# Optimization experiments

Hardware: AMD Instinct MI355X
Metric: run time of the kernel (lower is better)

## Reference

```python
import jax, jax.numpy as jnp
import numpy as np

B, T, S, H = 8, 256, 256, 512


def setup_inputs() -> dict:
    key = jax.random.key(0)
    k1, k2, k3, k4, k5, k6, k7 = jax.random.split(key, 7)
    query = jax.random.normal(k1, (B, T, H), dtype=jnp.float32)
    encoder_outputs = jax.random.normal(k2, (B, S, H), dtype=jnp.float32)
    src_lengths = jax.random.randint(k3, (B,), 1, S + 1)
    src_lengths = src_lengths.at[0].set(S)  # ensure max(lengths) == S (torch code masks to lengths.max())
    scale = 1.0 / np.sqrt(H)
    W_s = jax.random.normal(k4, (H, H), dtype=jnp.float32) * scale      # nn.Linear(H,H) weight
    W_h = jax.random.normal(k5, (H, H), dtype=jnp.float32) * scale
    v = jax.random.normal(k6, (H,), dtype=jnp.float32) * scale          # nn.Linear(H,1) weight
    W_out = jax.random.normal(k7, (H, 2 * H), dtype=jnp.float32) * scale  # nn.Linear(2H,H) weight
    return {"query": query, "encoder_outputs": encoder_outputs, "src_lengths": src_lengths,
            "W_s": W_s, "W_h": W_h, "v": v, "W_out": W_out}


def reference(query, encoder_outputs, src_lengths, W_s, W_h, v, W_out):
    # torch Linear: y = x @ W.T
    Ws_q = jnp.einsum('bth,oh->bto', query, W_s)            # (B,T,H)
    Wh_e = jnp.einsum('bsh,oh->bso', encoder_outputs, W_h)  # (B,S,H)
    # score(i,j) = v^T tanh(Ws_q_j + Wh_e_i), broadcast over (B,T,S,H)
    energies = jnp.einsum('btsh,h->bts',
                          jnp.tanh(Ws_q[:, :, None, :] + Wh_e[:, None, :, :]), v)
    mask = jnp.arange(encoder_outputs.shape[1]) < src_lengths[:, None]  # (B,S)
    energies = jnp.where(mask[:, None, :], energies, -jnp.inf)
    attn_weights = jax.nn.softmax(energies, axis=-1)        # (B,T,S)
    context = jnp.einsum('bts,bsh->bth', attn_weights, encoder_outputs)
    combined = jnp.concatenate([context, query], axis=-1)   # (B,T,2H)
    attn_out = jnp.tanh(jnp.einsum('btk,ok->bto', combined, W_out))
    return attn_out
```

## Files before the change

### kernel.cpp

```cpp
#include <hip/hip_runtime.h>
#include <hip/hip_bf16.h>


typedef __attribute__((ext_vector_type(8))) short bf16x8;
typedef __attribute__((ext_vector_type(4))) float floatx4;

#define C2LOG2E 2.8853900817779268f
#define LOG2E   1.4426950408889634f
#define NEGBIG  -1e30f

__device__ __forceinline__ float fexp2(float x) { return __builtin_amdgcn_exp2f(x); }
__device__ __forceinline__ float frcp(float x)  { return __builtin_amdgcn_rcpf(x); }
__device__ __forceinline__ float ftanh(float x) {
    return 1.0f - 2.0f * frcp(1.0f + fexp2(C2LOG2E * x));
}

__device__ __forceinline__ unsigned int f2bf_bits(float f) {
    unsigned int u = __float_as_uint(f);
    return (u + 0x7fffu + ((u >> 16) & 1u)) >> 16;
}

__global__ __launch_bounds__(256) void cast_all_bf16(
    const float* __restrict__ q,  const float* __restrict__ e,
    const float* __restrict__ Ws, const float* __restrict__ Wh,
    const float* __restrict__ Wo,
    unsigned short* __restrict__ qb,  unsigned short* __restrict__ eb,
    unsigned short* __restrict__ Wsb, unsigned short* __restrict__ Whb,
    unsigned short* __restrict__ Wob)
{
    int blk = blockIdx.x;
    const float* src; unsigned short* dst; int base;
    if      (blk < 1024) { src = q;  dst = qb;  base = blk; }
    else if (blk < 2048) { src = e;  dst = eb;  base = blk - 1024; }
    else if (blk < 2304) { src = Ws; dst = Wsb; base = blk - 2048; }
    else if (blk < 2560) { src = Wh; dst = Whb; base = blk - 2304; }
    else                 { src = Wo; dst = Wob; base = blk - 2560; }
    size_t i = (size_t)base * 1024 + threadIdx.x * 4;
    float4 f = *(const float4*)(src + i);
    ushort4 o;
    o.x = (unsigned short)f2bf_bits(f.x);
    o.y = (unsigned short)f2bf_bits(f.y);
    o.z = (unsigned short)f2bf_bits(f.z);
    o.w = (unsigned short)f2bf_bits(f.w);
    *(ushort4*)(dst + i) = o;
}

__global__ __launch_bounds__(256) void gemm32x64_tanh_dual(
    const unsigned short* __restrict__ Xa, const unsigned short* __restrict__ Wa,
    float* __restrict__ Ca,
    const unsigned short* __restrict__ Xb, const unsigned short* __restrict__ Wb_,
    float* __restrict__ Cb)
{
    __shared__ unsigned short sA[32 * 72];
    __shared__ unsigned short sB[64 * 72];
    const int K = 512;
    int blk = blockIdx.x;
    const unsigned short* X; const unsigned short* W; float* C;
    int mt, nt, N;
    if (blk < 512) { X = Xa; W = Wa; C = Ca; N = 512;  mt = blk >> 3; nt = blk & 7; }
    else { blk -= 512; X = Xb; W = Wb_; C = Cb; N = 2048; mt = blk >> 5; nt = blk & 31; }
    int row0 = mt * 32, col0 = nt * 64;
    int tid = threadIdx.x, lane = tid & 63, w = tid >> 6;
    int srA = tid >> 3, scA = (tid & 7) * 8;
    int srB = tid >> 2, scB = (tid & 3) * 16;
    int mw = (w & 1) * 16, nw = (w >> 1) * 32;
    int r = lane & 15, kq = (lane >> 4) * 8;

    floatx4 acc0 = {0,0,0,0}, acc1 = {0,0,0,0};
    const unsigned short* ga = X + (size_t)(row0 + srA) * K + scA;
    const unsigned short* gb = W + (size_t)(col0 + srB) * K + scB;

    for (int kb = 0; kb < 8; ++kb) {
        uint4 a0 = *(const uint4*)(ga);
        uint4 b0 = *(const uint4*)(gb);
        uint4 b1 = *(const uint4*)(gb + 8);
        ga += 64; gb += 64;
        __syncthreads();
        *(uint4*)&sA[srA * 72 + scA]     = a0;
        *(uint4*)&sB[srB * 72 + scB]     = b0;
        *(uint4*)&sB[srB * 72 + scB + 8] = b1;
        __syncthreads();
#pragma unroll
        for (int ks = 0; ks < 64; ks += 32) {
            bf16x8 af  = *(const bf16x8*)&sA[(mw + r) * 72 + ks + kq];
            bf16x8 bf0 = *(const bf16x8*)&sB[(nw + r) * 72 + ks + kq];
            bf16x8 bf1 = *(const bf16x8*)&sB[(nw + 16 + r) * 72 + ks + kq];
            acc0 = __builtin_amdgcn_mfma_f32_16x16x32_bf16(af, bf0, acc0, 0, 0, 0);
            acc1 = __builtin_amdgcn_mfma_f32_16x16x32_bf16(af, bf1, acc1, 0, 0, 0);
        }
    }
    int rq = (lane >> 4) * 4;
    float* cp = C + (size_t)(row0 + mw + rq) * N + col0 + nw + r;
#pragma unroll
    for (int i = 0; i < 4; ++i) {
        cp[(size_t)i * N]      = ftanh(acc0[i]);
        cp[(size_t)i * N + 16] = ftanh(acc1[i]);
    }
}

#define TQ 4
__global__ __launch_bounds__(512) void energies_softmax(
    const float* __restrict__ Aq,
    const float* __restrict__ BhT,
    const float* __restrict__ Vv,
    const int* __restrict__ Len,
    unsigned short* __restrict__ Wb)
{
    __shared__ float sA[TQ][512];
    __shared__ float sV[512];
    __shared__ float sRed[8][TQ][257];
    __shared__ float sE[TQ][256];

    int tid  = threadIdx.x;
    int lane = tid & 63;
    int w    = tid >> 6;
    int blk  = blockIdx.x;
    int b    = blk >> 6;
    int tq   = blk & 63;
    int row0g = b * 256 + tq * TQ;
    int len  = Len[b];
    int jmax = (len + 63) >> 6;

    {
        int idx = tid * 4, t = idx >> 9, c = idx & 511;
        *(float4*)&sA[t][c] = *(const float4*)(Aq + (size_t)(row0g + t) * 512 + c);
    }
    sV[tid] = Vv[tid];
    __syncthreads();

    int h0 = w * 64;
    float acc[TQ][4] = {{0.f}};
    const float* bt = BhT + (size_t)h0 * 2048 + b * 256 + lane;

#pragma unroll 2
    for (int hh = 0; hh < 64; hh += 4) {
        float Bv[4][4];
#pragma unroll
        for (int i = 0; i < 4; ++i)
#pragma unroll
            for (int j = 0; j < 4; ++j)
                if (j < jmax) Bv[i][j] = bt[(size_t)(hh + i) * 2048 + 64 * j];
        float4 v4 = *(const float4*)&sV[h0 + hh];
#pragma unroll
        for (int t = 0; t < TQ; ++t) {
            float4 a4 = *(const float4*)&sA[t][h0 + hh];
#pragma unroll
            for (int j = 0; j < 4; ++j) {
                if (j < jmax) {
                    float n0 = a4.x + Bv[0][j], n1 = a4.y + Bv[1][j];
                    float n2 = a4.z + Bv[2][j], n3 = a4.w + Bv[3][j];
                    float d0 = fmaf(a4.x, Bv[0][j], 1.0f), d1 = fmaf(a4.y, Bv[1][j], 1.0f);
                    float d2 = fmaf(a4.z, Bv[2][j], 1.0f), d3 = fmaf(a4.w, Bv[3][j], 1.0f);
                    float x0 = v4.x * n0, x1 = v4.y * n1;
                    float x2 = v4.z * n2, x3 = v4.w * n3;
                    float num01 = fmaf(x1, d0, x0 * d1);
                    float num23 = fmaf(x3, d2, x2 * d3);
                    acc[t][j] = fmaf(num01, frcp(d0 * d1), acc[t][j]);
                    acc[t][j] = fmaf(num23, frcp(d2 * d3), acc[t][j]);
                }
            }
        }
    }

#pragma unroll
    for (int t = 0; t < TQ; ++t)
#pragma unroll
        for (int j = 0; j < 4; ++j)
            sRed[w][t][lane + 64 * j] = acc[t][j];
    __syncthreads();
#pragma unroll
    for (int rep = 0; rep < 2; ++rep) {
        int p = tid + rep * 512;
        int t = p >> 8, s = p & 255;
        float sum = 0.f;
#pragma unroll
        for (int ww = 0; ww < 8; ++ww) sum += sRed[ww][t][s];
        sE[t][s] = sum;
    }
    __syncthreads();

    if (w < TQ) {
        float ev[4];
#pragma unroll
        for (int j = 0; j < 4; ++j) {
            int s = lane + 64 * j;
            ev[j] = (s < len) ? sE[w][s] : NEGBIG;
        }
        float m = fmaxf(fmaxf(ev[0], ev[1]), fmaxf(ev[2], ev[3]));
#pragma unroll
        for (int o = 1; o < 64; o <<= 1) m = fmaxf(m, __shfl_xor(m, o, 64));
        float wv[4], wsum = 0.f;
#pragma unroll
        for (int j = 0; j < 4; ++j) { wv[j] = fexp2((ev[j] - m) * LOG2E); wsum += wv[j]; }
#pragma unroll
        for (int o = 1; o < 64; o <<= 1) wsum += __shfl_xor(wsum, o, 64);
        float inv = frcp(wsum);
        unsigned short* wrow = Wb + (size_t)(row0g + w) * 256;
#pragma unroll
        for (int j = 0; j < 4; ++j)
            wrow[lane + 64 * j] = (unsigned short)f2bf_bits(wv[j] * inv);
    }
}

__global__ __launch_bounds__(512) void ctx_gemm(
    const unsigned short* __restrict__ Wbw,
    const unsigned short* __restrict__ Eb,
    unsigned short* __restrict__ Ctx)
{
    __shared__ unsigned short EncT[64][264];
    __shared__ unsigned short sWb[64][264];
    int tid = threadIdx.x, lane = tid & 63, w = tid >> 6;
    int blk = blockIdx.x;
    int b = blk & 7, hq = (blk >> 3) & 7, tg = blk >> 6;

    {
        int s = tid >> 1, hg = (tid & 1) * 32;
        const ushort4* src = (const ushort4*)(Eb + (size_t)(b * 256 + s) * 512 + hq * 64 + hg);
#pragma unroll
        for (int k = 0; k < 8; ++k) {
            ushort4 u = src[k];
            EncT[hg + k * 4 + 0][s] = u.x;
            EncT[hg + k * 4 + 1][s] = u.y;
            EncT[hg + k * 4 + 2][s] = u.z;
            EncT[hg + k * 4 + 3][s] = u.w;
        }
    }
    {
        int row = tid >> 3, seg = (tid & 7) * 32;
        const ushort4* src = (const ushort4*)(Wbw + (size_t)(b * 256 + tg * 64 + row) * 256 + seg);
        ushort4* dst = (ushort4*)&sWb[row][seg];
#pragma unroll
        for (int k = 0; k < 8; ++k) dst[k] = src[k];
    }
    __syncthreads();

    int mt = w & 3, npair = w >> 2;
    int t0 = mt * 16;
    int r  = lane & 15, kq = (lane >> 4) * 8;
    int n0 = npair * 32 + r;
    floatx4 acc0 = {0.f,0.f,0.f,0.f}, acc1 = {0.f,0.f,0.f,0.f};
#pragma unroll
    for (int k = 0; k < 8; ++k) {
        bf16x8 a  = *(const bf16x8*)(&sWb[t0 + r][kq + 32 * k]);
        bf16x8 b0 = *(const bf16x8*)(&EncT[n0][kq + 32 * k]);
        bf16x8 b1 = *(const bf16x8*)(&EncT[n0 + 16][kq + 32 * k]);
        acc0 = __builtin_amdgcn_mfma_f32_16x16x32_bf16(a, b0, acc0, 0, 0, 0);
        acc1 = __builtin_amdgcn_mfma_f32_16x16x32_bf16(a, b1, acc1, 0, 0, 0);
    }
    int row0 = (lane >> 4) * 4;
    unsigned short* op = Ctx + (size_t)(b * 256 + tg * 64 + t0 + row0) * 512 + hq * 64 + npair * 32 + r;
#pragma unroll
    for (int i = 0; i < 4; ++i) {
        op[i * 512]      = (unsigned short)f2bf_bits(acc0[i]);
        op[i * 512 + 16] = (unsigned short)f2bf_bits(acc1[i]);
    }
}

__global__ __launch_bounds__(256) void out_gemm32x64_tanh(
    const unsigned short* __restrict__ Ctx, const unsigned short* __restrict__ Q,
    const unsigned short* __restrict__ Wout, float* __restrict__ Out)
{
    __shared__ unsigned short sA[32 * 72];
    __shared__ unsigned short sB[64 * 72];
    const int N = 512, KW = 1024;
    int blk = blockIdx.x;
    int mt = blk >> 3, nt = blk & 7;
    int row0 = mt * 32, col0 = nt * 64;
    int tid = threadIdx.x, lane = tid & 63, w = tid >> 6;
    int srA = tid >> 3, scA = (tid & 7) * 8;
    int srB = tid >> 2, scB = (tid & 3) * 16;
    int mw = (w & 1) * 16, nw = (w >> 1) * 32;
    int r = lane & 15, kq = (lane >> 4) * 8;

    floatx4 acc0 = {0,0,0,0}, acc1 = {0,0,0,0};
    const unsigned short* gb = Wout + (size_t)(col0 + srB) * KW + scB;

    for (int kb = 0; kb < 16; ++kb) {
        const unsigned short* asrc = (kb < 8 ? Ctx : Q);
        const unsigned short* ga = asrc + (size_t)(row0 + srA) * 512 + (kb & 7) * 64 + scA;
        uint4 a0 = *(const uint4*)(ga);
        uint4 b0 = *(const uint4*)(gb);
        uint4 b1 = *(const uint4*)(gb + 8);
        gb += 64;
        __syncthreads();
        *(uint4*)&sA[srA * 72 + scA]     = a0;
        *(uint4*)&sB[srB * 72 + scB]     = b0;
        *(uint4*)&sB[srB * 72 + scB + 8] = b1;
        __syncthreads();
#pragma unroll
        for (int ks = 0; ks < 64; ks += 32) {
            bf16x8 af  = *(const bf16x8*)&sA[(mw + r) * 72 + ks + kq];
            bf16x8 bf0 = *(const bf16x8*)&sB[(nw + r) * 72 + ks + kq];
            bf16x8 bf1 = *(const bf16x8*)&sB[(nw + 16 + r) * 72 + ks + kq];
            acc0 = __builtin_amdgcn_mfma_f32_16x16x32_bf16(af, bf0, acc0, 0, 0, 0);
            acc1 = __builtin_amdgcn_mfma_f32_16x16x32_bf16(af, bf1, acc1, 0, 0, 0);
        }
    }
    int rq = (lane >> 4) * 4;
    float* op = Out + (size_t)(row0 + mw + rq) * N + col0 + nw + r;
#pragma unroll
    for (int i = 0; i < 4; ++i) {
        op[(size_t)i * N]      = ftanh(acc0[i]);
        op[(size_t)i * N + 16] = ftanh(acc1[i]);
    }
}

extern "C" void kernel_launch(void* const* d_in, const int* in_sizes, int n_in,
                              void* d_out, int out_size, void* d_ws, size_t ws_size,
                              hipStream_t stream)
{
    const float* query = (const float*)d_in[0];
    const float* enc   = (const float*)d_in[1];
    const int*   len   = (const int*)d_in[2];
    const float* Ws    = (const float*)d_in[3];
    const float* Wh    = (const float*)d_in[4];
    const float* v     = (const float*)d_in[5];
    const float* Wout  = (const float*)d_in[6];
    float* out = (float*)d_out;

    float* wsq  = (float*)d_ws;
    float* wheT = wsq + 2048 * 512;
    unsigned short* Wbw = (unsigned short*)(wheT + 512 * 2048);
    unsigned short* qb  = Wbw + 2048 * 256;
    unsigned short* eb  = qb + 2048 * 512;
    unsigned short* Wsb = eb + 2048 * 512;
    unsigned short* Whb = Wsb + 512 * 512;
    unsigned short* Wob = Whb + 512 * 512;
    unsigned short* ctx = Wob + 512 * 1024;

    cast_all_bf16<<<3072, 256, 0, stream>>>(query, enc, Ws, Wh, Wout,
                                            qb, eb, Wsb, Whb, Wob);
    gemm32x64_tanh_dual<<<1024, 256, 0, stream>>>(qb, Wsb, wsq, Whb, eb, wheT);
    energies_softmax<<<512, 512, 0, stream>>>(wsq, wheT, v, len, Wbw);
    ctx_gemm<<<256, 512, 0, stream>>>(Wbw, eb, ctx);
    out_gemm32x64_tanh<<<512, 256, 0, stream>>>(ctx, qb, Wob, out);
}
```

Measured before the change: 139.6 us.

## Split energies across source chunks and fuse softmax into context GEMM

The energies kernel now launches one block per (batch, query-tile, 64-wide source chunk), so there are four times as many blocks and fully masked chunks exit early. Each block reads query and v straight from global memory instead of staging them in shared memory, and it writes raw fp32 energies to a workspace. Softmax moves into the context GEMM kernel, which computes the bf16 weights directly into shared memory. The aim is more parallelism and less work per block in the energies stage. In exchange, the fp32 energies make a global round trip, and the softmax is recomputed in each of the 8 h-quarter blocks that share a query tile.

```diff
diff --git a/kernel.cpp b/kernel.cpp
--- a/kernel.cpp
+++ b/kernel.cpp
@@ -99,112 +99,72 @@
 }
 
 #define TQ 4
-__global__ __launch_bounds__(512) void energies_softmax(
+__global__ __launch_bounds__(512) void energies_reg(
     const float* __restrict__ Aq,
     const float* __restrict__ BhT,
     const float* __restrict__ Vv,
     const int* __restrict__ Len,
-    unsigned short* __restrict__ Wb)
-{
-    __shared__ float sA[TQ][512];
-    __shared__ float sV[512];
-    __shared__ float sRed[8][TQ][257];
-    __shared__ float sE[TQ][256];
+    float* __restrict__ E)
+{
+    __shared__ float sRed[8][TQ][66];
 
     int tid  = threadIdx.x;
     int lane = tid & 63;
     int w    = tid >> 6;
     int blk  = blockIdx.x;
-    int b    = blk >> 6;
+    int b    = blk >> 8;
+    int j    = (blk >> 6) & 3;
     int tq   = blk & 63;
+    int len  = Len[b];
+    if (j * 64 >= len) return;
     int row0g = b * 256 + tq * TQ;
-    int len  = Len[b];
-    int jmax = (len + 63) >> 6;
-
-    {
-        int idx = tid * 4, t = idx >> 9, c = idx & 511;
-        *(float4*)&sA[t][c] = *(const float4*)(Aq + (size_t)(row0g + t) * 512 + c);
-    }
-    sV[tid] = Vv[tid];
+
+    int h0 = __builtin_amdgcn_readfirstlane(w * 64);
+    const float* ap = Aq + (size_t)row0g * 512 + h0;
+    const float* vp = Vv + h0;
+
+    float acc[TQ] = {0.f, 0.f, 0.f, 0.f};
+    const float* bt = BhT + (size_t)h0 * 2048 + b * 256 + j * 64 + lane;
+
+#pragma unroll 4
+    for (int hh = 0; hh < 64; hh += 4) {
+        float B0 = bt[(size_t)(hh + 0) * 2048];
+        float B1 = bt[(size_t)(hh + 1) * 2048];
+        float B2 = bt[(size_t)(hh + 2) * 2048];
+        float B3 = bt[(size_t)(hh + 3) * 2048];
+        float4 v4 = *(const float4*)(vp + hh);
+#pragma unroll
+        for (int t = 0; t < TQ; ++t) {
+            float4 a4 = *(const float4*)(ap + t * 512 + hh);
+            float n0 = a4.x + B0, n1 = a4.y + B1;
+            float n2 = a4.z + B2, n3 = a4.w + B3;
+            float d0 = fmaf(a4.x, B0, 1.0f), d1 = fmaf(a4.y, B1, 1.0f);
+            float d2 = fmaf(a4.z, B2, 1.0f), d3 = fmaf(a4.w, B3, 1.0f);
+            float x0 = v4.x * n0, x1 = v4.y * n1;
+            float x2 = v4.z * n2, x3 = v4.w * n3;
+            float num01 = fmaf(x1, d0, x0 * d1);
+            float num23 = fmaf(x3, d2, x2 * d3);
+            acc[t] = fmaf(num01, frcp(d0 * d1), acc[t]);
+            acc[t] = fmaf(num23, frcp(d2 * d3), acc[t]);
+        }
+    }
+
+#pragma unroll
+    for (int t = 0; t < TQ; ++t) sRed[w][t][lane] = acc[t];
     __syncthreads();
-
-    int h0 = w * 64;
-    float acc[TQ][4] = {{0.f}};
-    const float* bt = BhT + (size_t)h0 * 2048 + b * 256 + lane;
-
-#pragma unroll 2
-    for (int hh = 0; hh < 64; hh += 4) {
-        float Bv[4][4];
-#pragma unroll
-        for (int i = 0; i < 4; ++i)
-#pragma unroll
-            for (int j = 0; j < 4; ++j)
-                if (j < jmax) Bv[i][j] = bt[(size_t)(hh + i) * 2048 + 64 * j];
-        float4 v4 = *(const float4*)&sV[h0 + hh];
-#pragma unroll
-        for (int t = 0; t < TQ; ++t) {
-            float4 a4 = *(const float4*)&sA[t][h0 + hh];
-#pragma unroll
-            for (int j = 0; j < 4; ++j) {
-                if (j < jmax) {
-                    float n0 = a4.x + Bv[0][j], n1 = a4.y + Bv[1][j];
-                    float n2 = a4.z + Bv[2][j], n3 = a4.w + Bv[3][j];
-                    float d0 = fmaf(a4.x, Bv[0][j], 1.0f), d1 = fmaf(a4.y, Bv[1][j], 1.0f);
-                    float d2 = fmaf(a4.z, Bv[2][j], 1.0f), d3 = fmaf(a4.w, Bv[3][j], 1.0f);
-                    float x0 = v4.x * n0, x1 = v4.y * n1;
-                    float x2 = v4.z * n2, x3 = v4.w * n3;
-                    float num01 = fmaf(x1, d0, x0 * d1);
-                    float num23 = fmaf(x3, d2, x2 * d3);
-                    acc[t][j] = fmaf(num01, frcp(d0 * d1), acc[t][j]);
-                    acc[t][j] = fmaf(num23, frcp(d2 * d3), acc[t][j]);
-                }
-            }
-        }
-    }
-
-#pragma unroll
-    for (int t = 0; t < TQ; ++t)
-#pragma unroll
-        for (int j = 0; j < 4; ++j)
-            sRed[w][t][lane + 64 * j] = acc[t][j];
-    __syncthreads();
-#pragma unroll
-    for (int rep = 0; rep < 2; ++rep) {
-        int p = tid + rep * 512;
-        int t = p >> 8, s = p & 255;
+    if (tid < 256) {
+        int t = tid >> 6, s = tid & 63;
         float sum = 0.f;
 #pragma unroll
         for (int ww = 0; ww < 8; ++ww) sum += sRed[ww][t][s];
-        sE[t][s] = sum;
-    }
-    __syncthreads();
-
-    if (w < TQ) {
-        float ev[4];
-#pragma unroll
-        for (int j = 0; j < 4; ++j) {
-            int s = lane + 64 * j;
-            ev[j] = (s < len) ? sE[w][s] : NEGBIG;
-        }
-        float m = fmaxf(fmaxf(ev[0], ev[1]), fmaxf(ev[2], ev[3]));
-#pragma unroll
-        for (int o = 1; o < 64; o <<= 1) m = fmaxf(m, __shfl_xor(m, o, 64));
-        float wv[4], wsum = 0.f;
-#pragma unroll
-        for (int j = 0; j < 4; ++j) { wv[j] = fexp2((ev[j] - m) * LOG2E); wsum += wv[j]; }
-#pragma unroll
-        for (int o = 1; o < 64; o <<= 1) wsum += __shfl_xor(wsum, o, 64);
-        float inv = frcp(wsum);
-        unsigned short* wrow = Wb + (size_t)(row0g + w) * 256;
-#pragma unroll
-        for (int j = 0; j < 4; ++j)
-            wrow[lane + 64 * j] = (unsigned short)f2bf_bits(wv[j] * inv);
-    }
-}
-
-__global__ __launch_bounds__(512) void ctx_gemm(
-    const unsigned short* __restrict__ Wbw,
+        E[(size_t)(row0g + t) * 256 + j * 64 + s] = sum;
+    }
+}
+
+__global__ __launch_bounds__(512) void softmax_ctx_fused(
+    const float* __restrict__ E,
     const unsigned short* __restrict__ Eb,
+    const int* __restrict__ Len,
     unsigned short* __restrict__ Ctx)
 {
     __shared__ unsigned short EncT[64][264];
@@ -212,6 +172,7 @@
     int tid = threadIdx.x, lane = tid & 63, w = tid >> 6;
     int blk = blockIdx.x;
     int b = blk & 7, hq = (blk >> 3) & 7, tg = blk >> 6;
+    int len = Len[b];
 
     {
         int s = tid >> 1, hg = (tid & 1) * 32;
@@ -225,12 +186,27 @@
             EncT[hg + k * 4 + 3][s] = u.w;
         }
     }
-    {
-        int row = tid >> 3, seg = (tid & 7) * 32;
-        const ushort4* src = (const ushort4*)(Wbw + (size_t)(b * 256 + tg * 64 + row) * 256 + seg);
-        ushort4* dst = (ushort4*)&sWb[row][seg];
-#pragma unroll
-        for (int k = 0; k < 8; ++k) dst[k] = src[k];
+    for (int i = 0; i < 8; ++i) {
+        int row = w * 8 + i;
+        const float* erow = E + (size_t)(b * 256 + tg * 64 + row) * 256;
+        float ev[4];
+#pragma unroll
+        for (int j = 0; j < 4; ++j) {
+            int s = lane + 64 * j;
+            ev[j] = (s < len) ? erow[s] : NEGBIG;
+        }
+        float m = fmaxf(fmaxf(ev[0], ev[1]), fmaxf(ev[2], ev[3]));
+#pragma unroll
+        for (int o = 1; o < 64; o <<= 1) m = fmaxf(m, __shfl_xor(m, o, 64));
+        float wv[4], wsum = 0.f;
+#pragma unroll
+        for (int j = 0; j < 4; ++j) { wv[j] = fexp2((ev[j] - m) * LOG2E); wsum += wv[j]; }
+#pragma unroll
+        for (int o = 1; o < 64; o <<= 1) wsum += __shfl_xor(wsum, o, 64);
+        float inv = frcp(wsum);
+#pragma unroll
+        for (int j = 0; j < 4; ++j)
+            sWb[row][lane + 64 * j] = (unsigned short)f2bf_bits(wv[j] * inv);
     }
     __syncthreads();
 
@@ -320,8 +296,8 @@
 
     float* wsq  = (float*)d_ws;
     float* wheT = wsq + 2048 * 512;
-    unsigned short* Wbw = (unsigned short*)(wheT + 512 * 2048);
-    unsigned short* qb  = Wbw + 2048 * 256;
+    float* E    = wheT + 512 * 2048;
+    unsigned short* qb  = (unsigned short*)(E + 2048 * 256);
     unsigned short* eb  = qb + 2048 * 512;
     unsigned short* Wsb = eb + 2048 * 512;
     unsigned short* Whb = Wsb + 512 * 512;
@@ -331,7 +307,7 @@
     cast_all_bf16<<<3072, 256, 0, stream>>>(query, enc, Ws, Wh, Wout,
                                             qb, eb, Wsb, Whb, Wob);
     gemm32x64_tanh_dual<<<1024, 256, 0, stream>>>(qb, Wsb, wsq, Whb, eb, wheT);
-    energies_softmax<<<512, 512, 0, stream>>>(wsq, wheT, v, len, Wbw);
-    ctx_gemm<<<256, 512, 0, stream>>>(Wbw, eb, ctx);
+    energies_reg<<<2048, 512, 0, stream>>>(wsq, wheT, v, len, E);
+    softmax_ctx_fused<<<256, 512, 0, stream>>>(E, eb, len, ctx);
     out_gemm32x64_tanh<<<512, 256, 0, stream>>>(ctx, qb, Wob, out);
 }
```

Result: faster. 133.4 us (-4.4%).
